# Optimization experiments

Measured on AMD Instinct MI355X. Metric: run time of the kernel, lower is better.

## Reference

```python
import jax, jax.numpy as jnp
import numpy as np
import math

L_LAYERS = 2; B = 2; SEQ = 1024; D = 512; N = 16; H = 8; DH = 64; P = 32; KC = 4; DTR = 32

def _silu(x):
    return x * jax.nn.sigmoid(x)

def _rms(x, w, eps=1e-6):
    return x * jax.lax.rsqrt(jnp.mean(x * x, axis=-1, keepdims=True) + eps) * w

def _mamba(x, Win, conv_w, conv_b, Wx, Wdt, bdt, Alog, Dp, Wout):
    # x: [b,l,d]; mamba-ssm reference math with expand=1 (d_inner == d)
    b, l, d = x.shape
    xz = x @ Win                                   # [b,l,2d]
    xc, z = jnp.split(xz, 2, axis=-1)
    xp = jnp.pad(xc, ((0, 0), (KC - 1, 0), (0, 0)))  # causal depthwise conv
    xc = sum(xp[:, k:k + l, :] * conv_w[:, k] for k in range(KC)) + conv_b
    xc = _silu(xc)
    dbl = xc @ Wx                                  # [b,l,dtr+2N]
    dt = dbl[..., :DTR]
    Bc = dbl[..., DTR:DTR + N]                     # [b,l,N]
    Cc = dbl[..., DTR + N:]                        # [b,l,N]
    dt = jax.nn.softplus(dt @ Wdt + bdt)           # [b,l,d]
    A = -jnp.exp(Alog)                             # [d,N]
    dA = jnp.exp(dt[..., None] * A)                # [b,l,d,N]
    dBu = dt[..., None] * Bc[:, :, None, :] * xc[..., None]  # [b,l,d,N]
    def step(h, inp):
        dA_t, dBu_t, C_t = inp
        h = dA_t * h + dBu_t                       # [b,d,N]
        return h, jnp.einsum('bdn,bn->bd', h, C_t)
    h0 = jnp.zeros((b, d, N), x.dtype)
    _, ys = jax.lax.scan(step, h0, (dA.transpose(1, 0, 2, 3), dBu.transpose(1, 0, 2, 3), Cc.transpose(1, 0, 2)))
    y = ys.transpose(1, 0, 2) + Dp * xc
    y = y * _silu(z)
    return y @ Wout

def _enformer_attn(q, k, vv, u, vb, w):
    # q,k,vv: [b,l,h,d]; u,vb: [h,d]; w: [h,d,P]
    b, l, h, d = q.shape
    Pd = w.shape[-1]
    pos = jnp.arange(l)
    dist = pos[None, :] - pos[:, None]             # [l,l]
    pow_rate = jnp.exp(jnp.log((l + 1) / 2.0) / (Pd // 2))
    cw = pow_rate ** jnp.arange(1, Pd // 2 + 1, dtype=jnp.float32)
    ub = (jnp.abs(dist)[:, :, None].astype(jnp.float32) <= cw)
    sb = jnp.sign(dist)[:, :, None].astype(jnp.float32) * ub.astype(jnp.float32)
    basis = jnp.concatenate([ub.astype(jnp.float32), sb], axis=-1)  # [l,l,P]
    scale = 1.0 / math.sqrt(d)
    # qr_term without materializing r[h,l,l,d]: (q@w) then contract with basis
    qw = jnp.einsum('bihd,hdn->bhin', q, w)
    qr = jnp.einsum('bhin,ijn->bhij', qw, basis)
    uk = jnp.einsum('hd,bjhd->bhj', u, k)[:, :, None, :]
    vr = jnp.einsum('hn,ijn->hij', jnp.einsum('hd,hdn->hn', vb, w), basis)
    scores = jnp.einsum('bihd,bjhd->bhij', q, k) * scale + (qr + uk + vr[None]) * scale
    attn = jax.nn.softmax(scores, axis=-1)
    return jnp.einsum('bhij,bjhd->bihd', attn, vv)

def _forward(x, rms_m, W_in, b_in, m_Win, m_conv_w, m_conv_b, m_Wx, m_Wdt, m_bdt, m_Alog, m_D, m_Wout, W_out, b_out, rms_a, Wq, Wk, Wv, u, v, w_rel, Wo, b_o):
    b, l, dm = x.shape
    for i in range(L_LAYERS):
        # --- BidirectionalMamba block (tie_in_proj=True, tie_gate=False) ---
        skip = x
        xn = _rms(x, rms_m[i])
        proj = xn @ W_in[i] + b_in[i]              # [b,l,3*dm]
        xf = proj[..., :dm]
        zf = proj[..., dm:2 * dm]
        zr = proj[..., 2 * dm:]
        yf = _mamba(xf, m_Win[i, 0], m_conv_w[i, 0], m_conv_b[i, 0], m_Wx[i, 0], m_Wdt[i, 0], m_bdt[i, 0], m_Alog[i, 0], m_D[i, 0], m_Wout[i, 0])
        yr = jnp.flip(_mamba(jnp.flip(xf, axis=1), m_Win[i, 1], m_conv_w[i, 1], m_conv_b[i, 1], m_Wx[i, 1], m_Wdt[i, 1], m_bdt[i, 1], m_Alog[i, 1], m_D[i, 1], m_Wout[i, 1]), axis=1)
        y = yf * _silu(zf) + yr * _silu(zr)
        x = y @ W_out[i] + b_out[i] + skip
        # --- Enformer relative-position attention block ---
        skip = x
        xn = _rms(x, rms_a[i])
        q = (xn @ Wq[i]).reshape(b, l, H, DH)
        k = (xn @ Wk[i]).reshape(b, l, H, DH)
        vv = (xn @ Wv[i]).reshape(b, l, H, DH)
        o = _enformer_attn(q, k, vv, u[i], v[i], w_rel[i]).reshape(b, l, H * DH)
        x = skip + o @ Wo[i] + b_o[i]
    return x

def setup_inputs() -> dict:
    key = jax.random.key(0)
    ks = iter(jax.random.split(key, 48))
    def rn(shape, s=0.02):
        return jax.random.normal(next(ks), shape, dtype=jnp.float32) * s
    L = L_LAYERS
    inp = {}
    inp['x'] = jax.random.normal(next(ks), (B, SEQ, D), dtype=jnp.float32)
    inp['rms_m'] = jnp.ones((L, D), jnp.float32)
    inp['W_in'] = rn((L, D, 3 * D)); inp['b_in'] = jnp.zeros((L, 3 * D), jnp.float32)
    inp['m_Win'] = rn((L, 2, D, 2 * D))
    inp['m_conv_w'] = rn((L, 2, D, KC), 0.1); inp['m_conv_b'] = jnp.zeros((L, 2, D), jnp.float32)
    inp['m_Wx'] = rn((L, 2, D, DTR + 2 * N))
    inp['m_Wdt'] = rn((L, 2, DTR, D), 0.1); inp['m_bdt'] = rn((L, 2, D), 0.5)
    inp['m_Alog'] = jnp.tile(jnp.log(jnp.arange(1, N + 1, dtype=jnp.float32)), (L, 2, D, 1))
    inp['m_D'] = jnp.ones((L, 2, D), jnp.float32)
    inp['m_Wout'] = rn((L, 2, D, D))
    inp['W_out'] = rn((L, D, D)); inp['b_out'] = jnp.zeros((L, D), jnp.float32)
    inp['rms_a'] = jnp.ones((L, D), jnp.float32)
    inp['Wq'] = rn((L, D, H * DH)); inp['Wk'] = rn((L, D, H * DH)); inp['Wv'] = rn((L, D, H * DH))
    inp['u'] = rn((L, H, DH), 0.1); inp['v'] = rn((L, H, DH), 0.1)
    inp['w_rel'] = rn((L, H, DH, P), 0.1)
    inp['Wo'] = rn((L, H * DH, D)); inp['b_o'] = jnp.zeros((L, D), jnp.float32)
    return inp

def reference(x, rms_m, W_in, b_in, m_Win, m_conv_w, m_conv_b, m_Wx, m_Wdt, m_bdt, m_Alog, m_D, m_Wout, W_out, b_out, rms_a, Wq, Wk, Wv, u, v, w_rel, Wo, b_o):
    return _forward(x, rms_m, W_in, b_in, m_Win, m_conv_w, m_conv_b, m_Wx, m_Wdt, m_bdt, m_Alog, m_D, m_Wout, W_out, b_out, rms_a, Wq, Wk, Wv, u, v, w_rel, Wo, b_o)
```

## Files before the change

kernel.cpp:

```cpp
#include <hip/hip_runtime.h>

#define LL 2
#define BB 2
#define SEQL 1024
#define DD 512
#define NN 16
#define HH 8
#define DHH 64
#define PPB 32
#define KCC 4
#define DTRR 32

#define GBS 4
#define TC 32
#define NC (SEQL / TC)
#define NR (GBS * DD * NN)
#define BHN (BB * HH * SEQL)

#define AR_L     4325376L
#define OFF_WIN  0L
#define OFF_MWIN 786432L
#define OFF_WT2  1835008L
#define OFF_MWOUT 2490368L
#define OFF_WOUT 3014656L
#define OFF_QKV  3276800L
#define OFF_WO   4063232L

typedef __attribute__((ext_vector_type(8))) short bf16x8;
typedef __attribute__((ext_vector_type(4))) short short4v;
typedef __attribute__((ext_vector_type(4))) float f32x4;

__device__ __forceinline__ float siluf(float x) { return x / (1.f + __expf(-x)); }
__device__ __forceinline__ float softplusf(float x) { return x > 20.f ? x : log1pf(__expf(x)); }

__device__ __forceinline__ unsigned short f2bf(float x) {
  union { float f; unsigned u; } v; v.f = x;
  unsigned r = v.u + 0x7fff + ((v.u >> 16) & 1);
  return (unsigned short)(r >> 16);
}

__device__ __forceinline__ bf16x8 ld_frag(const unsigned short* p) {
  short4v a = *(const short4v*)(p);
  short4v b = *(const short4v*)(p + 4);
  bf16x8 r;
  r[0]=a[0]; r[1]=a[1]; r[2]=a[2]; r[3]=a[3];
  r[4]=b[0]; r[5]=b[1]; r[6]=b[2]; r[7]=b[3];
  return r;
}

__device__ __forceinline__ bf16x8 pack8(const float* p) {
  bf16x8 r;
  #pragma unroll
  for (int e = 0; e < 8; e++) r[e] = (short)f2bf(p[e]);
  return r;
}

struct TD { const float* src; unsigned short* dst; int ldsrc; int K; int N; int t0; };
struct TDs { TD a[24]; };

__global__ __launch_bounds__(256) void wtrans_all(TDs ds)
{
  int bid = blockIdx.x;
  int mi = 0;
  #pragma unroll 1
  for (int i = 1; i < 24; i++) if (bid >= ds.a[i].t0) mi = i;
  TD d = ds.a[mi];
  int local = bid - d.t0;
  int tilesN = d.N >> 5;
  int tn = local % tilesN, tk = local / tilesN;
  __shared__ float t[32][33];
  int tx = threadIdx.x & 31, ty = threadIdx.x >> 5;
  int n0 = tn * 32, k0 = tk * 32;
  #pragma unroll
  for (int i = 0; i < 4; i++)
    t[ty + 8 * i][tx] = d.src[(long)(k0 + ty + 8 * i) * d.ldsrc + n0 + tx];
  __syncthreads();
  #pragma unroll
  for (int i = 0; i < 4; i++)
    d.dst[(long)(n0 + ty + 8 * i) * d.K + k0 + tx] = f2bf(t[tx][ty + 8 * i]);
}

__global__ __launch_bounds__(256) void weff_kernel(
    const float* __restrict__ Wx, const float* __restrict__ Wdt,
    unsigned short* __restrict__ WTA)
{
  int lg = blockIdx.z;
  int l = lg >> 1, g = lg & 1;
  const float* wx = Wx + (long)(l * 2 + g) * DD * 64;
  const float* wd = Wdt + (long)(l * 2 + g) * DTRR * DD;
  unsigned short* wt = WTA + (long)l * AR_L + OFF_WT2 + (long)g * 327680;
  int n0 = blockIdx.x * 32, k0 = blockIdx.y * 32;
  __shared__ float wx_s[32][33];
  __shared__ float wd_s[32][33];
  int tx = threadIdx.x & 31, ty = threadIdx.x >> 5;
  #pragma unroll
  for (int i = 0; i < 4; i++) {
    wx_s[ty + 8 * i][tx] = wx[(long)(k0 + ty + 8 * i) * 64 + tx];
    wd_s[ty + 8 * i][tx] = wd[(long)(ty + 8 * i) * DD + n0 + tx];
  }
  __syncthreads();
  #pragma unroll
  for (int i = 0; i < 4; i++) {
    int nl = ty + 8 * i;
    float s = 0.f;
    #pragma unroll
    for (int r = 0; r < 32; r++) s = fmaf(wx_s[tx][r], wd_s[r][nl], s);
    wt[(long)(n0 + nl) * DD + k0 + tx] = f2bf(s);
  }
}

__global__ __launch_bounds__(256) void rmsinv_kernel(
    const float* __restrict__ x, float* __restrict__ inv)
{
  int row = blockIdx.x * 4 + (threadIdx.x >> 6);
  int lane = threadIdx.x & 63;
  const float* xr = x + (long)row * DD;
  float4 a = *(const float4*)(xr + lane * 4);
  float4 b = *(const float4*)(xr + 256 + lane * 4);
  float s = a.x*a.x + a.y*a.y + a.z*a.z + a.w*a.w + b.x*b.x + b.y*b.y + b.z*b.z + b.w*b.w;
  for (int o = 32; o; o >>= 1) s += __shfl_down(s, o);
  if (lane == 0) inv[row] = rsqrtf(s / (float)DD + 1e-6f);
}

template<int BM, int BN>
__global__ __launch_bounds__(256) void gemm_bf16_t(
    const float* __restrict__ A, const unsigned short* __restrict__ WT,
    const float* __restrict__ bias, const float* __restrict__ resid,
    const float* __restrict__ invrow, const float* __restrict__ colw,
    float* __restrict__ C,
    int M, int N, int K, int lda, int ldc,
    long aBatch, long wBatch, long biasBatch, long cBatch,
    int aflipL, int act)
{
  constexpr int FM = BM / 32;
  constexpr int FN = BN / 32;
  int g = blockIdx.z;
  A  += (long)g * aBatch;
  WT += (long)g * wBatch;
  C  += (long)g * cBatch;
  if (bias) bias += (long)g * biasBatch;
  const bool flip = (aflipL > 0) && (g == 1);

  __shared__ unsigned short A_lds[BM][72];
  __shared__ unsigned short B_lds[BN][72];
  int tid = threadIdx.x;
  int w = tid >> 6, lane = tid & 63, li = lane & 15, lg = lane >> 4;
  int bm = blockIdx.y * BM, bn = blockIdx.x * BN;
  int wm = (w & 1) * (BM / 2), wn = (w >> 1) * (BN / 2);
  f32x4 acc[FM][FN] = {};

  const int kqA = (tid & 15) * 4, r0A = tid >> 4;
  const int kqB = (tid & 7) * 8,  r0B = tid >> 3;

  for (int k0 = 0; k0 < K; k0 += 64) {
    __syncthreads();
    float4 cw4 = {1.f, 1.f, 1.f, 1.f};
    if (colw) cw4 = *(const float4*)(colw + k0 + kqA);
    #pragma unroll
    for (int i = 0; i < BM / 16; i++) {
      int m = bm + r0A + 16 * i;
      int mm = m;
      if (flip) { int bb = m / aflipL; int t = m - bb * aflipL; mm = bb * aflipL + (aflipL - 1 - t); }
      float4 av = *(const float4*)(A + (long)mm * lda + k0 + kqA);
      float sc = invrow ? invrow[mm] : 1.f;
      short4v ap = { (short)f2bf(av.x * sc * cw4.x), (short)f2bf(av.y * sc * cw4.y),
                     (short)f2bf(av.z * sc * cw4.z), (short)f2bf(av.w * sc * cw4.w) };
      *(short4v*)(&A_lds[r0A + 16 * i][kqA]) = ap;
    }
    #pragma unroll
    for (int i = 0; i < BN / 32; i++) {
      int n = bn + r0B + 32 * i;
      bf16x8 bv = *(const bf16x8*)(WT + (long)n * K + k0 + kqB);
      *(bf16x8*)(&B_lds[r0B + 32 * i][kqB]) = bv;
    }
    __syncthreads();
    #pragma unroll
    for (int ks = 0; ks < 2; ks++) {
      bf16x8 af[FM], bfr[FN];
      #pragma unroll
      for (int fm = 0; fm < FM; fm++)
        af[fm] = *(const bf16x8*)(&A_lds[wm + fm * 16 + li][ks * 32 + lg * 8]);
      #pragma unroll
      for (int fn = 0; fn < FN; fn++)
        bfr[fn] = *(const bf16x8*)(&B_lds[wn + fn * 16 + li][ks * 32 + lg * 8]);
      #pragma unroll
      for (int fm = 0; fm < FM; fm++)
        #pragma unroll
        for (int fn = 0; fn < FN; fn++)
          acc[fm][fn] = __builtin_amdgcn_mfma_f32_16x16x32_bf16(af[fm], bfr[fn], acc[fm][fn], 0, 0, 0);
    }
  }
  #pragma unroll
  for (int fm = 0; fm < FM; fm++) {
    #pragma unroll
    for (int fn = 0; fn < FN; fn++) {
      int n = bn + wn + fn * 16 + li;
      float bv = bias ? bias[n] : 0.f;
      #pragma unroll
      for (int r = 0; r < 4; r++) {
        int m = bm + wm + fm * 16 + 4 * lg + r;
        float v = acc[fm][fn][r] + bv;
        if (act == 1) v = softplusf(v);
        if (resid) v += resid[(long)m * ldc + n];
        C[(long)m * ldc + n] = v;
      }
    }
  }
}

__global__ __launch_bounds__(256) void gemm_comb(
    const float* __restrict__ yp, const float* __restrict__ proj,
    const unsigned short* __restrict__ WT,
    const float* __restrict__ bias, const float* __restrict__ resid,
    float* __restrict__ C)
{
  __shared__ unsigned short A_lds[64][72];
  __shared__ unsigned short B_lds[64][72];
  int tid = threadIdx.x;
  int w = tid >> 6, lane = tid & 63, li = lane & 15, lg = lane >> 4;
  int bm = blockIdx.y * 64, bn = blockIdx.x * 64;
  int wm = (w & 1) * 32, wn = (w >> 1) * 32;
  f32x4 acc[2][2] = {};
  const long U = (long)BB * SEQL * DD;

  const int kqA = (tid & 15) * 4, r0A = tid >> 4;
  const int kqB = (tid & 7) * 8,  r0B = tid >> 3;

  for (int k0 = 0; k0 < DD; k0 += 64) {
    __syncthreads();
    #pragma unroll
    for (int i = 0; i < 4; i++) {
      int m = bm + r0A + 16 * i;
      int t = m & (SEQL - 1), b = m >> 10;
      int mf = (b << 10) + (SEQL - 1 - t);
      float4 y0 = *(const float4*)(yp + (long)m * DD + k0 + kqA);
      float4 y1 = *(const float4*)(yp + U + (long)mf * DD + k0 + kqA);
      float4 zf = *(const float4*)(proj + (long)m * 3 * DD + DD + k0 + kqA);
      float4 zr = *(const float4*)(proj + (long)m * 3 * DD + 2 * DD + k0 + kqA);
      float4 v;
      v.x = y0.x * siluf(zf.x) + y1.x * siluf(zr.x);
      v.y = y0.y * siluf(zf.y) + y1.y * siluf(zr.y);
      v.z = y0.z * siluf(zf.z) + y1.z * siluf(zr.z);
      v.w = y0.w * siluf(zf.w) + y1.w * siluf(zr.w);
      short4v ap = { (short)f2bf(v.x), (short)f2bf(v.y), (short)f2bf(v.z), (short)f2bf(v.w) };
      *(short4v*)(&A_lds[r0A + 16 * i][kqA]) = ap;
    }
    #pragma unroll
    for (int i = 0; i < 2; i++) {
      int n = bn + r0B + 32 * i;
      bf16x8 bv = *(const bf16x8*)(WT + (long)n * DD + k0 + kqB);
      *(bf16x8*)(&B_lds[r0B + 32 * i][kqB]) = bv;
    }
    __syncthreads();
    #pragma unroll
    for (int ks = 0; ks < 2; ks++) {
      bf16x8 af[2], bfr[2];
      #pragma unroll
      for (int fm = 0; fm < 2; fm++)
        af[fm] = *(const bf16x8*)(&A_lds[wm + fm * 16 + li][ks * 32 + lg * 8]);
      #pragma unroll
      for (int fn = 0; fn < 2; fn++)
        bfr[fn] = *(const bf16x8*)(&B_lds[wn + fn * 16 + li][ks * 32 + lg * 8]);
      #pragma unroll
      for (int fm = 0; fm < 2; fm++)
        #pragma unroll
        for (int fn = 0; fn < 2; fn++)
          acc[fm][fn] = __builtin_amdgcn_mfma_f32_16x16x32_bf16(af[fm], bfr[fn], acc[fm][fn], 0, 0, 0);
    }
  }
  #pragma unroll
  for (int fm = 0; fm < 2; fm++) {
    #pragma unroll
    for (int fn = 0; fn < 2; fn++) {
      int n = bn + wn + fn * 16 + li;
      float bv = bias[n];
      #pragma unroll
      for (int r = 0; r < 4; r++) {
        int m = bm + wm + fm * 16 + 4 * lg + r;
        C[(long)m * DD + n] = acc[fm][fn][r] + bv + resid[(long)m * DD + n];
      }
    }
  }
}

__global__ __launch_bounds__(256) void gemm_attn(
    const float* __restrict__ opart, const float* __restrict__ mbuf, const float* __restrict__ lbuf,
    const unsigned short* __restrict__ WT,
    const float* __restrict__ bias, const float* __restrict__ resid,
    float* __restrict__ C)
{
  __shared__ unsigned short A_lds[64][72];
  __shared__ unsigned short B_lds[64][72];
  int tid = threadIdx.x;
  int w = tid >> 6, lane = tid & 63, li = lane & 15, lg = lane >> 4;
  int bm = blockIdx.y * 64, bn = blockIdx.x * 64;
  int wm = (w & 1) * 32, wn = (w >> 1) * 32;
  f32x4 acc[2][2] = {};

  const int kqA = (tid & 15) * 4, r0A = tid >> 4;
  const int kqB = (tid & 7) * 8,  r0B = tid >> 3;

  for (int k0 = 0; k0 < DD; k0 += 64) {
    __syncthreads();
    int h = k0 >> 6;
    #pragma unroll
    for (int i = 0; i < 4; i++) {
      int m = bm + r0A + 16 * i;
      int iseq = m & (SEQL - 1), b = m >> 10;
      long row = ((long)(b * HH + h) << 10) + iseq;
      float m0 = mbuf[row], m1 = mbuf[BHN + row];
      float l0 = lbuf[row], l1 = lbuf[BHN + row];
      float mm = fmaxf(m0, m1);
      float e0 = __expf(m0 - mm), e1 = __expf(m1 - mm);
      float inv = 1.f / (l0 * e0 + l1 * e1);
      e0 *= inv; e1 *= inv;
      float4 o0 = *(const float4*)(opart + row * 64 + kqA);
      float4 o1 = *(const float4*)(opart + ((long)BHN + row) * 64 + kqA);
      float4 v;
      v.x = o0.x * e0 + o1.x * e1;
      v.y = o0.y * e0 + o1.y * e1;
      v.z = o0.z * e0 + o1.z * e1;
      v.w = o0.w * e0 + o1.w * e1;
      short4v ap = { (short)f2bf(v.x), (short)f2bf(v.y), (short)f2bf(v.z), (short)f2bf(v.w) };
      *(short4v*)(&A_lds[r0A + 16 * i][kqA]) = ap;
    }
    #pragma unroll
    for (int i = 0; i < 2; i++) {
      int n = bn + r0B + 32 * i;
      bf16x8 bv = *(const bf16x8*)(WT + (long)n * DD + k0 + kqB);
      *(bf16x8*)(&B_lds[r0B + 32 * i][kqB]) = bv;
    }
    __syncthreads();
    #pragma unroll
    for (int ks = 0; ks < 2; ks++) {
      bf16x8 af[2], bfr[2];
      #pragma unroll
      for (int fm = 0; fm < 2; fm++)
        af[fm] = *(const bf16x8*)(&A_lds[wm + fm * 16 + li][ks * 32 + lg * 8]);
      #pragma unroll
      for (int fn = 0; fn < 2; fn++)
        bfr[fn] = *(const bf16x8*)(&B_lds[wn + fn * 16 + li][ks * 32 + lg * 8]);
      #pragma unroll
      for (int fm = 0; fm < 2; fm++)
        #pragma unroll
        for (int fn = 0; fn < 2; fn++)
          acc[fm][fn] = __builtin_amdgcn_mfma_f32_16x16x32_bf16(af[fm], bfr[fn], acc[fm][fn], 0, 0, 0);
    }
  }
  #pragma unroll
  for (int fm = 0; fm < 2; fm++) {
    #pragma unroll
    for (int fn = 0; fn < 2; fn++) {
      int n = bn + wn + fn * 16 + li;
      float bv = bias[n];
      #pragma unroll
      for (int r = 0; r < 4; r++) {
        int m = bm + wm + fm * 16 + 4 * lg + r;
        C[(long)m * DD + n] = acc[fm][fn][r] + bv + resid[(long)m * DD + n];
      }
    }
  }
}

__global__ __launch_bounds__(256) void gemm_dtbc(
    const float* __restrict__ A, const unsigned short* __restrict__ WT2,
    const float* __restrict__ bdt, float* __restrict__ dtv, float* __restrict__ bc,
    int layer)
{
  int g = blockIdx.z;
  A   += (long)g * BB * SEQL * DD;
  WT2 += (long)g * 640 * DD;
  dtv += (long)g * BB * SEQL * DD;
  bc  += (long)g * BB * SEQL * 32;
  bdt += (long)(layer * 2 + g) * DD;

  __shared__ unsigned short A_lds[64][72];
  __shared__ unsigned short B_lds[64][72];
  int tid = threadIdx.x;
  int w = tid >> 6, lane = tid & 63, li = lane & 15, lg = lane >> 4;
  int bm = blockIdx.y * 64, bn = blockIdx.x * 64;
  int wm = (w & 1) * 32, wn = (w >> 1) * 32;
  f32x4 acc[2][2] = {};

  const int kqA = (tid & 15) * 4, r0A = tid >> 4;
  const int kqB = (tid & 7) * 8,  r0B = tid >> 3;

  for (int k0 = 0; k0 < DD; k0 += 64) {
    __syncthreads();
    #pragma unroll
    for (int i = 0; i < 4; i++) {
      int m = bm + r0A + 16 * i;
      float4 av = *(const float4*)(A + (long)m * DD + k0 + kqA);
      short4v ap = { (short)f2bf(av.x), (short)f2bf(av.y), (short)f2bf(av.z), (short)f2bf(av.w) };
      *(short4v*)(&A_lds[r0A + 16 * i][kqA]) = ap;
    }
    #pragma unroll
    for (int i = 0; i < 2; i++) {
      int n = bn + r0B + 32 * i;
      bf16x8 bv = *(const bf16x8*)(WT2 + (long)n * DD + k0 + kqB);
      *(bf16x8*)(&B_lds[r0B + 32 * i][kqB]) = bv;
    }
    __syncthreads();
    #pragma unroll
    for (int ks = 0; ks < 2; ks++) {
      bf16x8 af[2], bfr[2];
      #pragma unroll
      for (int fm = 0; fm < 2; fm++)
        af[fm] = *(const bf16x8*)(&A_lds[wm + fm * 16 + li][ks * 32 + lg * 8]);
      #pragma unroll
      for (int fn = 0; fn < 2; fn++)
        bfr[fn] = *(const bf16x8*)(&B_lds[wn + fn * 16 + li][ks * 32 + lg * 8]);
      #pragma unroll
      for (int fm = 0; fm < 2; fm++)
        #pragma unroll
        for (int fn = 0; fn < 2; fn++)
          acc[fm][fn] = __builtin_amdgcn_mfma_f32_16x16x32_bf16(af[fm], bfr[fn], acc[fm][fn], 0, 0, 0);
    }
  }
  #pragma unroll
  for (int fm = 0; fm < 2; fm++) {
    #pragma unroll
    for (int fn = 0; fn < 2; fn++) {
      int n = bn + wn + fn * 16 + li;
      if (n < 512) {
        float bv = bdt[n];
        #pragma unroll
        for (int r = 0; r < 4; r++) {
          int m = bm + wm + fm * 16 + 4 * lg + r;
          dtv[(long)m * DD + n] = softplusf(acc[fm][fn][r] + bv);
        }
      } else if (n < 544) {
        #pragma unroll
        for (int r = 0; r < 4; r++) {
          int m = bm + wm + fm * 16 + 4 * lg + r;
          bc[(long)m * 32 + (n - 512)] = acc[fm][fn][r];
        }
      }
    }
  }
}

__global__ __launch_bounds__(256) void conv_silu_kernel(
    const float* __restrict__ xz, const float* __restrict__ cw, const float* __restrict__ cb,
    float* __restrict__ xc, int layer)
{
  long idx = (long)blockIdx.x * 256 + threadIdx.x;
  int c = idx % DD;
  long r = idx / DD;
  int t = r % SEQL;
  long gb = r / SEQL;
  int g = (int)(gb / BB);
  const float* w = cw + ((long)(layer * 2 + g) * DD + c) * KCC;
  float acc = cb[(long)(layer * 2 + g) * DD + c];
  const float* xp = xz + (r - t) * 2 * DD + c;
  #pragma unroll
  for (int k = 0; k < KCC; k++) {
    int tt = t - (KCC - 1) + k;
    if (tt >= 0) acc = fmaf(xp[(long)tt * 2 * DD], w[k], acc);
  }
  xc[idx] = siluf(acc);
}

__global__ __launch_bounds__(256) void scan_chunk_kernel(
    const float* __restrict__ dtv, const float* __restrict__ xc,
    const float* __restrict__ bc, const float* __restrict__ Alog,
    float* __restrict__ P, float* __restrict__ Hend, int layer)
{
  int chunk = blockIdx.x, dtile = blockIdx.y, gb = blockIdx.z;
  int g = gb / BB;
  int tid = threadIdx.x;
  int dl = tid >> 1, nh = (tid & 1) * 8;
  int d = dtile * 128 + dl;
  int t0 = chunk * TC;
  __shared__ float dtv_s[TC][128], xc_s[TC][128], BC_s[TC][32];
  {
    long base = ((long)gb * SEQL + t0) * DD + dtile * 128;
    int c4 = (tid & 31) * 4, r0 = tid >> 5;
    #pragma unroll
    for (int i = 0; i < 4; i++) {
      int tl = r0 + i * 8;
      *(float4*)&dtv_s[tl][c4] = *(const float4*)(dtv + base + (long)tl * DD + c4);
      *(float4*)&xc_s[tl][c4]  = *(const float4*)(xc + base + (long)tl * DD + c4);
    }
    long dbase = ((long)gb * SEQL + t0) * 32;
    int cc = (tid & 7) * 4, rr = tid >> 3;
    *(float4*)&BC_s[rr][cc] = *(const float4*)(bc + dbase + (long)rr * 32 + cc);
  }
  __syncthreads();
  const float* Al = Alog + ((long)((layer * 2 + g) * DD) + d) * NN + nh;
  float a[8], h[8] = {};
  #pragma unroll
  for (int n = 0; n < 8; n++) a[n] = -__expf(Al[n]);
  float sdt = 0.f;
  for (int t = 0; t < TC; t++) {
    float dt = dtv_s[t][dl];
    float dx = dt * xc_s[t][dl];
    float4 b0 = *(const float4*)&BC_s[t][nh];
    float4 b1 = *(const float4*)&BC_s[t][nh + 4];
    h[0] = fmaf(__expf(dt * a[0]), h[0], dx * b0.x);
    h[1] = fmaf(__expf(dt * a[1]), h[1], dx * b0.y);
    h[2] = fmaf(__expf(dt * a[2]), h[2], dx * b0.z);
    h[3] = fmaf(__expf(dt * a[3]), h[3], dx * b0.w);
    h[4] = fmaf(__expf(dt * a[4]), h[4], dx * b1.x);
    h[5] = fmaf(__expf(dt * a[5]), h[5], dx * b1.y);
    h[6] = fmaf(__expf(dt * a[6]), h[6], dx * b1.z);
    h[7] = fmaf(__expf(dt * a[7]), h[7], dx * b1.w);
    sdt += dt;
  }
  long o = (long)chunk * NR + ((long)(gb * DD + d)) * NN + nh;
  #pragma unroll
  for (int n = 0; n < 8; n++) {
    P[o + n] = __expf(a[n] * sdt);
    Hend[o + n] = h[n];
  }
}

__global__ __launch_bounds__(256) void scan_combine_kernel(
    const float* __restrict__ P, const float* __restrict__ Hend, float* __restrict__ Hin)
{
  int r = blockIdx.x * 256 + threadIdx.x;
  float h = 0.f;
  #pragma unroll
  for (int c = 0; c < NC; c++) {
    Hin[(long)c * NR + r] = h;
    h = fmaf(P[(long)c * NR + r], h, Hend[(long)c * NR + r]);
  }
}

__global__ __launch_bounds__(256) void scan_apply_kernel(
    const float* __restrict__ dtv, const float* __restrict__ xc, const float* __restrict__ xz,
    const float* __restrict__ bc, const float* __restrict__ Alog, const float* __restrict__ Dp,
    const float* __restrict__ Hin, float* __restrict__ ym, int layer)
{
  int chunk = blockIdx.x, dtile = blockIdx.y, gb = blockIdx.z;
  int g = gb / BB;
  int tid = threadIdx.x;
  int dl = tid >> 1, nh = (tid & 1) * 8;
  int d = dtile * 128 + dl;
  int t0 = chunk * TC;
  __shared__ float dtv_s[TC][128], xc_s[TC][128], BC_s[TC][32], y_s[TC][128];
  {
    long base = ((long)gb * SEQL + t0) * DD + dtile * 128;
    int c4 = (tid & 31) * 4, r0 = tid >> 5;
    #pragma unroll
    for (int i = 0; i < 4; i++) {
      int tl = r0 + i * 8;
      *(float4*)&dtv_s[tl][c4] = *(const float4*)(dtv + base + (long)tl * DD + c4);
      *(float4*)&xc_s[tl][c4]  = *(const float4*)(xc + base + (long)tl * DD + c4);
    }
    long dbase = ((long)gb * SEQL + t0) * 32;
    int cc = (tid & 7) * 4, rr = tid >> 3;
    *(float4*)&BC_s[rr][cc] = *(const float4*)(bc + dbase + (long)rr * 32 + cc);
  }
  __syncthreads();
  const float* Al = Alog + ((long)((layer * 2 + g) * DD) + d) * NN + nh;
  float a[8], h[8];
  #pragma unroll
  for (int n = 0; n < 8; n++) a[n] = -__expf(Al[n]);
  {
    long r = (long)chunk * NR + ((long)(gb * DD + d)) * NN + nh;
    float4 h0 = *(const float4*)(Hin + r);
    float4 h1 = *(const float4*)(Hin + r + 4);
    h[0]=h0.x; h[1]=h0.y; h[2]=h0.z; h[3]=h0.w;
    h[4]=h1.x; h[5]=h1.y; h[6]=h1.z; h[7]=h1.w;
  }
  for (int t = 0; t < TC; t++) {
    float dt = dtv_s[t][dl];
    float dx = dt * xc_s[t][dl];
    float4 b0 = *(const float4*)&BC_s[t][nh];
    float4 b1 = *(const float4*)&BC_s[t][nh + 4];
    float4 c0 = *(const float4*)&BC_s[t][16 + nh];
    float4 c1 = *(const float4*)&BC_s[t][16 + nh + 4];
    h[0] = fmaf(__expf(dt * a[0]), h[0], dx * b0.x);
    h[1] = fmaf(__expf(dt * a[1]), h[1], dx * b0.y);
    h[2] = fmaf(__expf(dt * a[2]), h[2], dx * b0.z);
    h[3] = fmaf(__expf(dt * a[3]), h[3], dx * b0.w);
    h[4] = fmaf(__expf(dt * a[4]), h[4], dx * b1.x);
    h[5] = fmaf(__expf(dt * a[5]), h[5], dx * b1.y);
    h[6] = fmaf(__expf(dt * a[6]), h[6], dx * b1.z);
    h[7] = fmaf(__expf(dt * a[7]), h[7], dx * b1.w);
    float v0 = h[0] * c0.x + h[1] * c0.y;
    float v1 = h[2] * c0.z + h[3] * c0.w;
    float v2 = h[4] * c1.x + h[5] * c1.y;
    float v3 = h[6] * c1.z + h[7] * c1.w;
    float val = (v0 + v1) + (v2 + v3);
    val += __shfl_xor(val, 1);
    if ((tid & 1) == 0) y_s[t][dl] = val;
  }
  __syncthreads();
  {
    long base = ((long)gb * SEQL + t0) * DD + dtile * 128;
    long zbase = ((long)gb * SEQL + t0) * 2 * DD + DD + dtile * 128;
    int c4 = (tid & 31) * 4, r0 = tid >> 5;
    float4 Dp4 = *(const float4*)(Dp + (long)(layer * 2 + g) * DD + dtile * 128 + c4);
    #pragma unroll
    for (int i = 0; i < 4; i++) {
      int tl = r0 + i * 8;
      float4 y4 = *(const float4*)&y_s[tl][c4];
      float4 x4 = *(const float4*)&xc_s[tl][c4];
      float4 z4 = *(const float4*)(xz + zbase + (long)tl * 2 * DD + c4);
      float4 o;
      o.x = (y4.x + Dp4.x * x4.x) * siluf(z4.x);
      o.y = (y4.y + Dp4.y * x4.y) * siluf(z4.y);
      o.z = (y4.z + Dp4.z * x4.z) * siluf(z4.z);
      o.w = (y4.w + Dp4.w * x4.w) * siluf(z4.w);
      *(float4*)(ym + base + (long)tl * DD + c4) = o;
    }
  }
}

__global__ void tab_kernel(unsigned short* __restrict__ tab)
{
  int idx = blockIdx.x * blockDim.x + threadIdx.x;
  if (idx >= 2047) return;
  int di = idx - 1023;
  int ad = di < 0 ? -di : di;
  float pr = expf(logf((SEQL + 1) * 0.5f) / 16.0f);
  int n0 = 16;
  for (int n = 15; n >= 0; n--) {
    float cw = powf(pr, (float)(n + 1));
    if ((float)ad <= cw) n0 = n;
  }
  tab[idx] = (unsigned short)(di == 0 ? 34 : (di < 0 ? n0 : 17 + n0));
}

__global__ __launch_bounds__(256) void qw_kernel(
    const float* __restrict__ q, const float* __restrict__ w_rel, float* __restrict__ S, int layer)
{
  int itile = blockIdx.x;
  int bh = blockIdx.y;
  int h = bh % HH, b = bh / HH;
  int i0 = itile * 64;
  __shared__ float q_s[64][65];
  __shared__ float w_s[64][33];
  __shared__ float qwn[64][33];
  int tid = threadIdx.x;
  {
    int r = tid >> 2, c4 = (tid & 3) * 16;
    const float* qr = q + ((long)(b * SEQL + i0 + r)) * DD + h * 64 + c4;
    #pragma unroll
    for (int e = 0; e < 4; e++) {
      float4 v = *(const float4*)(qr + e * 4);
      q_s[r][c4 + e * 4 + 0] = v.x; q_s[r][c4 + e * 4 + 1] = v.y;
      q_s[r][c4 + e * 4 + 2] = v.z; q_s[r][c4 + e * 4 + 3] = v.w;
    }
  }
  for (int idx = tid; idx < 64 * 32; idx += 256) {
    int d = idx >> 5, n = idx & 31;
    w_s[d][n] = w_rel[((long)(layer * HH + h) * DHH + d) * PPB + n];
  }
  __syncthreads();
  {
    int i = tid & 63, ngrp = tid >> 6;
    float acc[8] = {};
    #pragma unroll 8
    for (int d = 0; d < 64; d++) {
      float qv = q_s[i][d];
      #pragma unroll
      for (int e = 0; e < 8; e++) acc[e] = fmaf(qv, w_s[d][ngrp * 8 + e], acc[e]);
    }
    #pragma unroll
    for (int e = 0; e < 8; e++) qwn[i][ngrp * 8 + e] = acc[e];
  }
  __syncthreads();
  for (int idx = tid; idx < 64 * 17; idx += 256) {
    int il = idx / 17, m = idx % 17;
    float s1 = 0.f, s2 = 0.f;
    for (int n = m; n < 16; n++) { s1 += qwn[il][n]; s2 += qwn[il][16 + n]; }
    float* Sp = S + ((long)bh * SEQL + i0 + il) * 34;
    Sp[m] = s1;
    Sp[17 + m] = s2;
  }
}

__global__ __launch_bounds__(256) void vw_kernel(
    const float* __restrict__ vparam, const float* __restrict__ w_rel, float* __restrict__ VS)
{
  int layer = blockIdx.x;
  __shared__ float vws[HH][PPB];
  int tid = threadIdx.x;
  int h = tid / PPB, n = tid % PPB;
  const float* vp = vparam + (long)(layer * HH + h) * DHH;
  const float* wp = w_rel + ((long)(layer * HH + h) * DHH) * PPB + n;
  float s = 0.f;
  for (int d = 0; d < DHH; d++) s = fmaf(vp[d], wp[d * PPB], s);
  vws[h][n] = s;
  __syncthreads();
  if (tid < HH * 17) {
    int hh = tid / 17, m = tid % 17;
    float s1 = 0.f, s2 = 0.f;
    for (int nn = m; nn < 16; nn++) { s1 += vws[hh][nn]; s2 += vws[hh][16 + nn]; }
    VS[layer * 272 + hh * 34 + m] = s1;
    VS[layer * 272 + hh * 34 + 17 + m] = s2;
  }
}

__global__ __launch_bounds__(256) void kvprep_kernel(
    const float* __restrict__ k, const float* __restrict__ v, const float* __restrict__ u,
    unsigned short* __restrict__ kbf, unsigned short* __restrict__ vtbf,
    float* __restrict__ uk, int layer)
{
  int itile = blockIdx.x;
  int bh = blockIdx.y;
  int h = bh & 7, b = bh >> 3;
  int i0 = itile * 64;
  int tid = threadIdx.x;
  __shared__ float vt_s[64][65];
  int r = tid >> 2, dseg = (tid & 3) * 16;
  const float* krow = k + ((long)(b * SEQL + i0 + r)) * DD + h * 64 + dseg;
  const float* vrow = v + ((long)(b * SEQL + i0 + r)) * DD + h * 64 + dseg;
  const float* urow = u + (long)(layer * HH + h) * DHH + dseg;
  unsigned short* kb = kbf + ((long)bh * SEQL + i0 + r) * 64 + dseg;
  float dot = 0.f;
  #pragma unroll
  for (int e = 0; e < 4; e++) {
    float4 kv = *(const float4*)(krow + e * 4);
    short4v kp = { (short)f2bf(kv.x), (short)f2bf(kv.y), (short)f2bf(kv.z), (short)f2bf(kv.w) };
    *(short4v*)(kb + e * 4) = kp;
    float4 uv = *(const float4*)(urow + e * 4);
    dot += kv.x * uv.x + kv.y * uv.y + kv.z * uv.z + kv.w * uv.w;
    float4 vv4 = *(const float4*)(vrow + e * 4);
    vt_s[dseg + e * 4 + 0][r] = vv4.x;
    vt_s[dseg + e * 4 + 1][r] = vv4.y;
    vt_s[dseg + e * 4 + 2][r] = vv4.z;
    vt_s[dseg + e * 4 + 3][r] = vv4.w;
  }
  dot += __shfl_xor(dot, 1);
  dot += __shfl_xor(dot, 2);
  if ((tid & 3) == 0) uk[(long)bh * SEQL + i0 + r] = dot;
  __syncthreads();
  int d = tid >> 2, jseg = (tid & 3) * 16;
  unsigned short* vt = vtbf + ((long)bh * 64 + d) * SEQL + i0 + jseg;
  #pragma unroll
  for (int e = 0; e < 4; e++) {
    short4v vp = { (short)f2bf(vt_s[d][jseg + e * 4 + 0]),
                   (short)f2bf(vt_s[d][jseg + e * 4 + 1]),
                   (short)f2bf(vt_s[d][jseg + e * 4 + 2]),
                   (short)f2bf(vt_s[d][jseg + e * 4 + 3]) };
    *(short4v*)(vt + e * 4) = vp;
  }
}

__global__ __launch_bounds__(256) void attn_mfma_kernel(
    const float* __restrict__ q, const unsigned short* __restrict__ kbf,
    const unsigned short* __restrict__ vtbf,
    const float* __restrict__ S, const float* __restrict__ VS, const float* __restrict__ uk,
    const unsigned short* __restrict__ tab,
    float* __restrict__ opart, float* __restrict__ mbuf, float* __restrict__ lbuf)
{
  __shared__ __align__(16) char smem[39680];
  unsigned short* K_lds  = (unsigned short*)(smem);
  unsigned short* VT_lds = (unsigned short*)(smem + 8704);
  unsigned short* PT_lds = (unsigned short*)(smem + 17408);
  float* E               = (float*)(smem + 26112);
  unsigned short* tab_s  = (unsigned short*)(smem + 35328);
  float* uk_s            = (float*)(smem + 39424);
  float* O_lds           = (float*)(smem);

  int itile = blockIdx.x;
  int bh = blockIdx.y;
  int split = blockIdx.z;
  int h = bh % HH, b = bh / HH;
  int i0 = itile * 64;
  int tid = threadIdx.x;
  int w = tid >> 6;
  int lane = tid & 63;
  int li = lane & 15, lg = lane >> 4;

  for (int idx = tid; idx < 64 * 17; idx += 256) {
    int il = idx / 17, m = idx % 17;
    long srow = ((long)bh * SEQL + i0 + il) * 34;
    float c0 = S[srow + m]      + VS[h * 34 + m];
    float c1 = S[srow + 17 + m] + VS[h * 34 + 17 + m];
    E[il * 36 + m]      = c0 - c1;
    E[il * 36 + 17 + m] = c0 + c1;
    if (m == 0) E[il * 36 + 34] = c0;
  }
  for (int idx = tid; idx < 2047; idx += 256) tab_s[idx] = tab[idx];

  int iq = i0 + w * 16 + li;
  const float* qrow = q + ((long)(b * SEQL + iq)) * DD + h * 64;
  bf16x8 qf0 = pack8(qrow + 8 * lg);
  bf16x8 qf1 = pack8(qrow + 32 + 8 * lg);

  f32x4 oacc[4] = {};
  float mrun = -1e30f, lrun = 0.f;
  const int ibase = i0 + w * 16 + li;
  unsigned short* PTw = PT_lds + w * 16 * 68;
  const float* Erow = E + (w * 16 + li) * 36;

  const int stR = tid >> 2, stS = (tid & 3) * 16;

  const int jbase = split * (SEQL / 2);
  for (int jt = 0; jt < SEQL / 2; jt += 64) {
    int j0 = jbase + jt;
    __syncthreads();
    {
      const unsigned short* ksrc = kbf + ((long)bh * SEQL + j0 + stR) * 64 + stS;
      *(bf16x8*)(K_lds + stR * 68 + stS)     = *(const bf16x8*)(ksrc);
      *(bf16x8*)(K_lds + stR * 68 + stS + 8) = *(const bf16x8*)(ksrc + 8);
      const unsigned short* vsrc = vtbf + ((long)bh * 64 + stR) * SEQL + j0 + stS;
      *(bf16x8*)(VT_lds + stR * 68 + stS)     = *(const bf16x8*)(vsrc);
      *(bf16x8*)(VT_lds + stR * 68 + stS + 8) = *(const bf16x8*)(vsrc + 8);
      if (tid < 64) uk_s[tid] = uk[(long)bh * SEQL + j0 + tid];
    }
    __syncthreads();

    f32x4 sf[4];
    #pragma unroll
    for (int jj = 0; jj < 4; jj++) {
      f32x4 c = {};
      c = __builtin_amdgcn_mfma_f32_16x16x32_bf16(
            ld_frag(K_lds + (jj * 16 + li) * 68 + 8 * lg), qf0, c, 0, 0, 0);
      c = __builtin_amdgcn_mfma_f32_16x16x32_bf16(
            ld_frag(K_lds + (jj * 16 + li) * 68 + 32 + 8 * lg), qf1, c, 0, 0, 0);
      sf[jj] = c;
    }

    float sv[4][4];
    float tmax = -1e30f;
    #pragma unroll
    for (int jj = 0; jj < 4; jj++) {
      #pragma unroll
      for (int r = 0; r < 4; r++) {
        int jloc = jj * 16 + 4 * lg + r;
        int di = (j0 + jloc) - ibase;
        int id = tab_s[1023 + di];
        float val = (sf[jj][r] + Erow[id] + uk_s[jloc]) * 0.125f;
        sv[jj][r] = val;
        tmax = fmaxf(tmax, val);
      }
    }
    tmax = fmaxf(tmax, __shfl_xor(tmax, 16));
    tmax = fmaxf(tmax, __shfl_xor(tmax, 32));
    float mnew = fmaxf(mrun, tmax);
    float fsc = __expf(mrun - mnew);
    mrun = mnew;
    lrun *= fsc;
    #pragma unroll
    for (int df = 0; df < 4; df++) oacc[df] *= fsc;

    float psum = 0.f;
    #pragma unroll
    for (int jj = 0; jj < 4; jj++) {
      short4v pk;
      #pragma unroll
      for (int r = 0; r < 4; r++) {
        float p = __expf(sv[jj][r] - mnew);
        psum += p;
        pk[r] = (short)f2bf(p);
      }
      *(short4v*)(PTw + li * 68 + jj * 16 + 4 * lg) = pk;
    }
    psum += __shfl_xor(psum, 16);
    psum += __shfl_xor(psum, 32);
    lrun += psum;

    asm volatile("s_waitcnt lgkmcnt(0)" ::: "memory");

    bf16x8 pf0 = ld_frag(PTw + li * 68 + 8 * lg);
    bf16x8 pf1 = ld_frag(PTw + li * 68 + 32 + 8 * lg);
    #pragma unroll
    for (int df = 0; df < 4; df++) {
      f32x4 c = oacc[df];
      c = __builtin_amdgcn_mfma_f32_16x16x32_bf16(
            ld_frag(VT_lds + (df * 16 + li) * 68 + 8 * lg), pf0, c, 0, 0, 0);
      c = __builtin_amdgcn_mfma_f32_16x16x32_bf16(
            ld_frag(VT_lds + (df * 16 + li) * 68 + 32 + 8 * lg), pf1, c, 0, 0, 0);
      oacc[df] = c;
    }
  }

  __syncthreads();
  if (lg == 0) {
    long row = (long)split * BHN + (long)bh * SEQL + (i0 + w * 16 + li);
    mbuf[row] = mrun;
    lbuf[row] = lrun;
  }
  #pragma unroll
  for (int df = 0; df < 4; df++)
    *(f32x4*)(O_lds + (w * 16 + li) * 68 + df * 16 + 4 * lg) = oacc[df];
  __syncthreads();
  {
    int il = tid >> 2, c0 = (tid & 3) * 16;
    long orow = ((long)split * BHN + (long)bh * SEQL + i0 + il) * 64 + c0;
    #pragma unroll
    for (int c4 = 0; c4 < 4; c4++) {
      f32x4 o = *(const f32x4*)(O_lds + il * 68 + c0 + c4 * 4);
      *(f32x4*)(opart + orow + c4 * 4) = o;
    }
  }
}

extern "C" void kernel_launch(void* const* d_in, const int* in_sizes, int n_in,
                              void* d_out, int out_size, void* d_ws, size_t ws_size,
                              hipStream_t stream) {
  const float* x_in     = (const float*)d_in[0];
  const float* rms_m    = (const float*)d_in[1];
  const float* W_in     = (const float*)d_in[2];
  const float* b_in     = (const float*)d_in[3];
  const float* m_Win    = (const float*)d_in[4];
  const float* m_conv_w = (const float*)d_in[5];
  const float* m_conv_b = (const float*)d_in[6];
  const float* m_Wx     = (const float*)d_in[7];
  const float* m_Wdt    = (const float*)d_in[8];
  const float* m_bdt    = (const float*)d_in[9];
  const float* m_Alog   = (const float*)d_in[10];
  const float* m_Dp     = (const float*)d_in[11];
  const float* m_Wout   = (const float*)d_in[12];
  const float* W_out    = (const float*)d_in[13];
  const float* b_out    = (const float*)d_in[14];
  const float* rms_a    = (const float*)d_in[15];
  const float* Wq       = (const float*)d_in[16];
  const float* Wk       = (const float*)d_in[17];
  const float* Wv       = (const float*)d_in[18];
  const float* u_p      = (const float*)d_in[19];
  const float* v_p      = (const float*)d_in[20];
  const float* w_rel    = (const float*)d_in[21];
  const float* Wo       = (const float*)d_in[22];
  const float* b_o      = (const float*)d_in[23];
  float* out = (float*)d_out;

  float* ws = (float*)d_ws;
  const long U = (long)BB * SEQL * DD;
  float* xA    = ws;
  float* xB    = ws + 1 * U;
  float* xn    = ws + 2 * U;
  float* proj  = ws + 3 * U;
  float* xz    = ws + 6 * U;
  float* xc    = ws + 10 * U;
  float* dtv   = ws + 12 * U;
  float* ym    = ws + 14 * U;
  float* ycomb = ws + 16 * U;
  float* smallb= ws + 17 * U;
  float* bcbuf = smallb;
  float* ukbuf = smallb + 262144;
  float* Sbuf  = smallb + 278528;
  float* VSbuf = smallb + 835584;
  unsigned short* tabg = (unsigned short*)(smallb + 836880);
  float* invm  = smallb + 838928;
  float* inva  = smallb + 840976;
  unsigned short* WTA = (unsigned short*)(ws + 18 * U);
  float* yp = xz;
  float* qb = proj;
  float* kb = proj + U;
  float* vb = proj + 2 * U;
  float* Pbuf = xn;
  float* Hend = xB;
  float* Hin  = ycomb;
  float* opart = xc;
  float* mbuf  = dtv;
  float* lbuf  = dtv + 2 * BHN;
  unsigned short* kbf  = (unsigned short*)ym;
  unsigned short* vtbf = kbf + (long)BHN * 64;

  const int M = BB * SEQL;

  tab_kernel<<<8, 256, 0, stream>>>(tabg);

  TDs td;
  int cum = 0, idx = 0;
  auto add = [&](const float* s, unsigned short* dst, int ldsrc, int K, int N) {
    td.a[idx].src = s; td.a[idx].dst = dst; td.a[idx].ldsrc = ldsrc;
    td.a[idx].K = K; td.a[idx].N = N; td.a[idx].t0 = cum;
    cum += (N / 32) * (K / 32); idx++;
  };
  for (int l = 0; l < LL; l++) {
    unsigned short* base = WTA + (long)l * AR_L;
    add(W_in   + (long)l * DD * 3 * DD,        base + OFF_WIN,            3 * DD, DD, 3 * DD);
    add(m_Win  + (long)(l * 2 + 0) * DD * 2 * DD, base + OFF_MWIN,          2 * DD, DD, 2 * DD);
    add(m_Win  + (long)(l * 2 + 1) * DD * 2 * DD, base + OFF_MWIN + 524288, 2 * DD, DD, 2 * DD);
    add(m_Wout + (long)(l * 2 + 0) * DD * DD,  base + OFF_MWOUT,          DD, DD, DD);
    add(m_Wout + (long)(l * 2 + 1) * DD * DD,  base + OFF_MWOUT + 262144, DD, DD, DD);
    add(W_out  + (long)l * DD * DD,            base + OFF_WOUT,           DD, DD, DD);
    add(Wq     + (long)l * DD * DD,            base + OFF_QKV,            DD, DD, DD);
    add(Wk     + (long)l * DD * DD,            base + OFF_QKV + 262144,   DD, DD, DD);
    add(Wv     + (long)l * DD * DD,            base + OFF_QKV + 524288,   DD, DD, DD);
    add(Wo     + (long)l * DD * DD,            base + OFF_WO,             DD, DD, DD);
    add(m_Wx   + (long)(l * 2 + 0) * DD * 64 + 32, base + OFF_WT2 + 262144,          64, DD, 32);
    add(m_Wx   + (long)(l * 2 + 1) * DD * 64 + 32, base + OFF_WT2 + 327680 + 262144, 64, DD, 32);
  }
  wtrans_all<<<cum, 256, 0, stream>>>(td);
  weff_kernel<<<dim3(16, 16, 2 * LL), 256, 0, stream>>>(m_Wx, m_Wdt, WTA);
  vw_kernel<<<LL, 256, 0, stream>>>(v_p, w_rel, VSbuf);

  for (int layer = 0; layer < LL; layer++) {
    const float* cur = (layer == 0) ? x_in : xA;
    unsigned short* base = WTA + (long)layer * AR_L;
    rmsinv_kernel<<<M / 4, 256, 0, stream>>>(cur, invm);
    gemm_bf16_t<64, 64><<<dim3(24, 32, 1), 256, 0, stream>>>(cur, base + OFF_WIN,
        b_in + layer * 3 * DD, nullptr, invm, rms_m + layer * DD, proj,
        M, 3 * DD, DD, DD, 3 * DD, 0, 0, 0, 0, 0, 0);
    gemm_bf16_t<64, 64><<<dim3(16, 32, 2), 256, 0, stream>>>(proj, base + OFF_MWIN,
        nullptr, nullptr, nullptr, nullptr, xz, M, 2 * DD, DD, 3 * DD, 2 * DD,
        0, 524288, 0, (long)BB * SEQL * 2 * DD, SEQL, 0);
    conv_silu_kernel<<<(2 * BB * SEQL * DD) / 256, 256, 0, stream>>>(xz, m_conv_w, m_conv_b, xc, layer);
    gemm_dtbc<<<dim3(9, 32, 2), 256, 0, stream>>>(xc, base + OFF_WT2, m_bdt, dtv, bcbuf, layer);
    scan_chunk_kernel<<<dim3(NC, DD / 128, GBS), 256, 0, stream>>>(
        dtv, xc, bcbuf, m_Alog, Pbuf, Hend, layer);
    scan_combine_kernel<<<NR / 256, 256, 0, stream>>>(Pbuf, Hend, Hin);
    scan_apply_kernel<<<dim3(NC, DD / 128, GBS), 256, 0, stream>>>(
        dtv, xc, xz, bcbuf, m_Alog, m_Dp, Hin, ym, layer);
    gemm_bf16_t<64, 64><<<dim3(8, 32, 2), 256, 0, stream>>>(ym, base + OFF_MWOUT,
        nullptr, nullptr, nullptr, nullptr, yp, M, DD, DD, DD, DD,
        U, 262144, 0, U, 0, 0);
    gemm_comb<<<dim3(8, 32), 256, 0, stream>>>(yp, proj, base + OFF_WOUT,
        b_out + layer * DD, cur, xB);

    rmsinv_kernel<<<M / 4, 256, 0, stream>>>(xB, inva);
    gemm_bf16_t<64, 64><<<dim3(8, 32, 3), 256, 0, stream>>>(xB, base + OFF_QKV,
        nullptr, nullptr, inva, rms_a + layer * DD, qb, M, DD, DD, DD, DD,
        0, 262144, 0, U, 0, 0);
    qw_kernel<<<dim3(16, 16), 256, 0, stream>>>(qb, w_rel, Sbuf, layer);
    kvprep_kernel<<<dim3(16, 16), 256, 0, stream>>>(kb, vb, u_p, kbf, vtbf, ukbuf, layer);
    attn_mfma_kernel<<<dim3(SEQL / 64, BB * HH, 2), 256, 0, stream>>>(
        qb, kbf, vtbf, Sbuf, VSbuf + layer * 272, ukbuf, tabg, opart, mbuf, lbuf);

    float* outp = (layer == LL - 1) ? out : xA;
    gemm_attn<<<dim3(8, 32), 256, 0, stream>>>(opart, mbuf, lbuf, base + OFF_WO,
        b_o + layer * DD, xB, outp);
  }
}
```

Before: 556.6 us.

## Fuse K/V bf16 conversion into QKV GEMM epilogue and split attention four ways

```diff
diff --git a/kernel.cpp b/kernel.cpp
--- a/kernel.cpp
+++ b/kernel.cpp
@@ -16,6 +16,7 @@
 #define NC (SEQL / TC)
 #define NR (GBS * DD * NN)
 #define BHN (BB * HH * SEQL)
+#define NSPLIT 4
 
 #define AR_L     4325376L
 #define OFF_WIN  0L
@@ -205,6 +206,119 @@
         C[(long)m * ldc + n] = v;
       }
     }
+  }
+}
+
+__global__ __launch_bounds__(256) void gemm_qkv(
+    const float* __restrict__ A, const unsigned short* __restrict__ WT,
+    const float* __restrict__ invrow, const float* __restrict__ colw,
+    const float* __restrict__ u_p,
+    float* __restrict__ qb, unsigned short* __restrict__ kbf,
+    unsigned short* __restrict__ vtbf, float* __restrict__ uk, int layer)
+{
+  int g = blockIdx.z;
+  WT += (long)g * 262144;
+
+  __shared__ unsigned short A_lds[64][72];
+  __shared__ unsigned short B_lds[64][72];
+  __shared__ float ukp[64][2];
+  int tid = threadIdx.x;
+  int w = tid >> 6, lane = tid & 63, li = lane & 15, lg = lane >> 4;
+  int bm = blockIdx.y * 64, bn = blockIdx.x * 64;
+  int wm = (w & 1) * 32, wn = (w >> 1) * 32;
+  f32x4 acc[2][2] = {};
+
+  const int kqA = (tid & 15) * 4, r0A = tid >> 4;
+  const int kqB = (tid & 7) * 8,  r0B = tid >> 3;
+
+  for (int k0 = 0; k0 < DD; k0 += 64) {
+    __syncthreads();
+    float4 cw4 = *(const float4*)(colw + k0 + kqA);
+    #pragma unroll
+    for (int i = 0; i < 4; i++) {
+      int m = bm + r0A + 16 * i;
+      float4 av = *(const float4*)(A + (long)m * DD + k0 + kqA);
+      float sc = invrow[m];
+      short4v ap = { (short)f2bf(av.x * sc * cw4.x), (short)f2bf(av.y * sc * cw4.y),
+                     (short)f2bf(av.z * sc * cw4.z), (short)f2bf(av.w * sc * cw4.w) };
+      *(short4v*)(&A_lds[r0A + 16 * i][kqA]) = ap;
+    }
+    #pragma unroll
+    for (int i = 0; i < 2; i++) {
+      int n = bn + r0B + 32 * i;
+      bf16x8 bv = *(const bf16x8*)(WT + (long)n * DD + k0 + kqB);
+      *(bf16x8*)(&B_lds[r0B + 32 * i][kqB]) = bv;
+    }
+    __syncthreads();
+    #pragma unroll
+    for (int ks = 0; ks < 2; ks++) {
+      bf16x8 af[2], bfr[2];
+      #pragma unroll
+      for (int fm = 0; fm < 2; fm++)
+        af[fm] = *(const bf16x8*)(&A_lds[wm + fm * 16 + li][ks * 32 + lg * 8]);
+      #pragma unroll
+      for (int fn = 0; fn < 2; fn++)
+        bfr[fn] = *(const bf16x8*)(&B_lds[wn + fn * 16 + li][ks * 32 + lg * 8]);
+      #pragma unroll
+      for (int fm = 0; fm < 2; fm++)
+        #pragma unroll
+        for (int fn = 0; fn < 2; fn++)
+          acc[fm][fn] = __builtin_amdgcn_mfma_f32_16x16x32_bf16(af[fm], bfr[fn], acc[fm][fn], 0, 0, 0);
+    }
+  }
+
+  int h = blockIdx.x;
+  int b = bm >> 10;
+  long bh = b * HH + h;
+  if (g == 0) {
+    #pragma unroll
+    for (int fm = 0; fm < 2; fm++)
+      #pragma unroll
+      for (int fn = 0; fn < 2; fn++) {
+        int n = bn + wn + fn * 16 + li;
+        #pragma unroll
+        for (int r = 0; r < 4; r++) {
+          int m = bm + wm + fm * 16 + 4 * lg + r;
+          qb[(long)m * DD + n] = acc[fm][fn][r];
+        }
+      }
+  } else if (g == 1) {
+    float u0 = u_p[(long)(layer * HH + h) * DHH + wn + li];
+    float u1 = u_p[(long)(layer * HH + h) * DHH + wn + 16 + li];
+    #pragma unroll
+    for (int fm = 0; fm < 2; fm++) {
+      #pragma unroll
+      for (int r = 0; r < 4; r++) {
+        int m = bm + wm + fm * 16 + 4 * lg + r;
+        int i = m & (SEQL - 1);
+        unsigned short* kr = kbf + (bh * SEQL + i) * 64 + wn;
+        kr[li]      = f2bf(acc[fm][0][r]);
+        kr[16 + li] = f2bf(acc[fm][1][r]);
+        float part = acc[fm][0][r] * u0 + acc[fm][1][r] * u1;
+        part += __shfl_xor(part, 1);
+        part += __shfl_xor(part, 2);
+        part += __shfl_xor(part, 4);
+        part += __shfl_xor(part, 8);
+        if (li == 0) ukp[wm + fm * 16 + 4 * lg + r][w >> 1] = part;
+      }
+    }
+    __syncthreads();
+    if (tid < 64) {
+      int i = (bm + tid) & (SEQL - 1);
+      uk[bh * SEQL + i] = ukp[tid][0] + ukp[tid][1];
+    }
+  } else {
+    #pragma unroll
+    for (int fm = 0; fm < 2; fm++)
+      #pragma unroll
+      for (int fn = 0; fn < 2; fn++) {
+        int d = wn + fn * 16 + li;
+        int m0 = bm + wm + fm * 16 + 4 * lg;
+        int i0 = m0 & (SEQL - 1);
+        short4v vp = { (short)f2bf(acc[fm][fn][0]), (short)f2bf(acc[fm][fn][1]),
+                       (short)f2bf(acc[fm][fn][2]), (short)f2bf(acc[fm][fn][3]) };
+        *(short4v*)(vtbf + (bh * 64 + d) * SEQL + i0) = vp;
+      }
   }
 }
 
@@ -308,19 +422,28 @@
       int m = bm + r0A + 16 * i;
       int iseq = m & (SEQL - 1), b = m >> 10;
       long row = ((long)(b * HH + h) << 10) + iseq;
-      float m0 = mbuf[row], m1 = mbuf[BHN + row];
-      float l0 = lbuf[row], l1 = lbuf[BHN + row];
-      float mm = fmaxf(m0, m1);
-      float e0 = __expf(m0 - mm), e1 = __expf(m1 - mm);
-      float inv = 1.f / (l0 * e0 + l1 * e1);
-      e0 *= inv; e1 *= inv;
-      float4 o0 = *(const float4*)(opart + row * 64 + kqA);
-      float4 o1 = *(const float4*)(opart + ((long)BHN + row) * 64 + kqA);
-      float4 v;
-      v.x = o0.x * e0 + o1.x * e1;
-      v.y = o0.y * e0 + o1.y * e1;
-      v.z = o0.z * e0 + o1.z * e1;
-      v.w = o0.w * e0 + o1.w * e1;
+      float ms[NSPLIT], ls[NSPLIT];
+      float mm = -1e30f;
+      #pragma unroll
+      for (int s = 0; s < NSPLIT; s++) {
+        ms[s] = mbuf[(long)s * BHN + row];
+        ls[s] = lbuf[(long)s * BHN + row];
+        mm = fmaxf(mm, ms[s]);
+      }
+      float den = 0.f, es[NSPLIT];
+      #pragma unroll
+      for (int s = 0; s < NSPLIT; s++) {
+        es[s] = __expf(ms[s] - mm);
+        den += ls[s] * es[s];
+      }
+      float inv = 1.f / den;
+      float4 v = {0.f, 0.f, 0.f, 0.f};
+      #pragma unroll
+      for (int s = 0; s < NSPLIT; s++) {
+        float e = es[s] * inv;
+        float4 o = *(const float4*)(opart + ((long)s * BHN + row) * 64 + kqA);
+        v.x += o.x * e; v.y += o.y * e; v.z += o.z * e; v.w += o.w * e;
+      }
       short4v ap = { (short)f2bf(v.x), (short)f2bf(v.y), (short)f2bf(v.z), (short)f2bf(v.w) };
       *(short4v*)(&A_lds[r0A + 16 * i][kqA]) = ap;
     }
@@ -695,52 +818,6 @@
   }
 }
 
-__global__ __launch_bounds__(256) void kvprep_kernel(
-    const float* __restrict__ k, const float* __restrict__ v, const float* __restrict__ u,
-    unsigned short* __restrict__ kbf, unsigned short* __restrict__ vtbf,
-    float* __restrict__ uk, int layer)
-{
-  int itile = blockIdx.x;
-  int bh = blockIdx.y;
-  int h = bh & 7, b = bh >> 3;
-  int i0 = itile * 64;
-  int tid = threadIdx.x;
-  __shared__ float vt_s[64][65];
-  int r = tid >> 2, dseg = (tid & 3) * 16;
-  const float* krow = k + ((long)(b * SEQL + i0 + r)) * DD + h * 64 + dseg;
-  const float* vrow = v + ((long)(b * SEQL + i0 + r)) * DD + h * 64 + dseg;
-  const float* urow = u + (long)(layer * HH + h) * DHH + dseg;
-  unsigned short* kb = kbf + ((long)bh * SEQL + i0 + r) * 64 + dseg;
-  float dot = 0.f;
-  #pragma unroll
-  for (int e = 0; e < 4; e++) {
-    float4 kv = *(const float4*)(krow + e * 4);
-    short4v kp = { (short)f2bf(kv.x), (short)f2bf(kv.y), (short)f2bf(kv.z), (short)f2bf(kv.w) };
-    *(short4v*)(kb + e * 4) = kp;
-    float4 uv = *(const float4*)(urow + e * 4);
-    dot += kv.x * uv.x + kv.y * uv.y + kv.z * uv.z + kv.w * uv.w;
-    float4 vv4 = *(const float4*)(vrow + e * 4);
-    vt_s[dseg + e * 4 + 0][r] = vv4.x;
-    vt_s[dseg + e * 4 + 1][r] = vv4.y;
-    vt_s[dseg + e * 4 + 2][r] = vv4.z;
-    vt_s[dseg + e * 4 + 3][r] = vv4.w;
-  }
-  dot += __shfl_xor(dot, 1);
-  dot += __shfl_xor(dot, 2);
-  if ((tid & 3) == 0) uk[(long)bh * SEQL + i0 + r] = dot;
-  __syncthreads();
-  int d = tid >> 2, jseg = (tid & 3) * 16;
-  unsigned short* vt = vtbf + ((long)bh * 64 + d) * SEQL + i0 + jseg;
-  #pragma unroll
-  for (int e = 0; e < 4; e++) {
-    short4v vp = { (short)f2bf(vt_s[d][jseg + e * 4 + 0]),
-                   (short)f2bf(vt_s[d][jseg + e * 4 + 1]),
-                   (short)f2bf(vt_s[d][jseg + e * 4 + 2]),
-                   (short)f2bf(vt_s[d][jseg + e * 4 + 3]) };
-    *(short4v*)(vt + e * 4) = vp;
-  }
-}
-
 __global__ __launch_bounds__(256) void attn_mfma_kernel(
     const float* __restrict__ q, const unsigned short* __restrict__ kbf,
     const unsigned short* __restrict__ vtbf,
@@ -791,8 +868,8 @@
 
   const int stR = tid >> 2, stS = (tid & 3) * 16;
 
-  const int jbase = split * (SEQL / 2);
-  for (int jt = 0; jt < SEQL / 2; jt += 64) {
+  const int jbase = split * (SEQL / NSPLIT);
+  for (int jt = 0; jt < SEQL / NSPLIT; jt += 64) {
     int j0 = jbase + jt;
     __syncthreads();
     {
@@ -943,14 +1020,12 @@
   unsigned short* WTA = (unsigned short*)(ws + 18 * U);
   float* yp = xz;
   float* qb = proj;
-  float* kb = proj + U;
-  float* vb = proj + 2 * U;
   float* Pbuf = xn;
   float* Hend = xB;
   float* Hin  = ycomb;
-  float* opart = xc;
+  float* opart = ws + 8 * U;
   float* mbuf  = dtv;
-  float* lbuf  = dtv + 2 * BHN;
+  float* lbuf  = dtv + NSPLIT * BHN;
   unsigned short* kbf  = (unsigned short*)ym;
   unsigned short* vtbf = kbf + (long)BHN * 64;
 
@@ -1008,12 +1083,10 @@
         b_out + layer * DD, cur, xB);
 
     rmsinv_kernel<<<M / 4, 256, 0, stream>>>(xB, inva);
-    gemm_bf16_t<64, 64><<<dim3(8, 32, 3), 256, 0, stream>>>(xB, base + OFF_QKV,
-        nullptr, nullptr, inva, rms_a + layer * DD, qb, M, DD, DD, DD, DD,
-        0, 262144, 0, U, 0, 0);
+    gemm_qkv<<<dim3(8, 32, 3), 256, 0, stream>>>(xB, base + OFF_QKV,
+        inva, rms_a + layer * DD, u_p, qb, kbf, vtbf, ukbuf, layer);
     qw_kernel<<<dim3(16, 16), 256, 0, stream>>>(qb, w_rel, Sbuf, layer);
-    kvprep_kernel<<<dim3(16, 16), 256, 0, stream>>>(kb, vb, u_p, kbf, vtbf, ukbuf, layer);
-    attn_mfma_kernel<<<dim3(SEQL / 64, BB * HH, 2), 256, 0, stream>>>(
+    attn_mfma_kernel<<<dim3(SEQL / 64, BB * HH, NSPLIT), 256, 0, stream>>>(
         qb, kbf, vtbf, Sbuf, VSbuf + layer * 272, ukbuf, tabg, opart, mbuf, lbuf);
 
     float* outp = (layer == LL - 1) ? out : xA;
```

Result: slower. 581.5 us (+4.5%).
